# Kernel optimization log

Measured on AMD Instinct MI355X. Metric: run time of the kernel, lower is better.

Reference implementation:

```python
import jax, jax.numpy as jnp
import numpy as np

H = 56; W = 56; WS = 7; SHIFT = 3; HEADS = 4; DIM = 128
N = WS * WS  # 49 tokens per window
EPS = 1e-5


def _rel_pos_index():
    c = np.stack(np.meshgrid(np.arange(WS), np.arange(WS), indexing='ij')).reshape(2, -1)
    r = (c[:, :, None] - c[:, None, :]).transpose(1, 2, 0)
    r[..., 0] += WS - 1
    r[..., 1] += WS - 1
    r[..., 0] *= 2 * WS - 1
    return jnp.asarray(r.sum(-1))  # [N, N] int


def _attn_mask():
    img = np.zeros((H, W))
    sl = (slice(0, -WS), slice(-WS, -SHIFT), slice(-SHIFT, None))
    cnt = 0
    for hs in sl:
        for ws_ in sl:
            img[hs, ws_] = cnt
            cnt += 1
    mw = img.reshape(H // WS, WS, W // WS, WS).transpose(0, 2, 1, 3).reshape(-1, N)
    d = mw[:, None, :] - mw[:, :, None]  # [nW, N, N]
    return jnp.asarray(np.where(d != 0, -100.0, 0.0).astype(np.float32))


def _ln(x, w, b):
    m = x.mean(-1, keepdims=True)
    v = ((x - m) ** 2).mean(-1, keepdims=True)
    return (x - m) / jnp.sqrt(v + EPS) * w + b


def setup_inputs() -> dict:
    key = jax.random.key(0)
    ks = jax.random.split(key, 8)
    B = 64
    return {
        'x': jax.random.normal(ks[0], (B, H * W, DIM), jnp.float32),
        'qkv_w': jax.random.normal(ks[1], (DIM, 3 * DIM), jnp.float32) * 0.02,
        'qkv_b': jnp.zeros((3 * DIM,), jnp.float32),
        'proj_w': jax.random.normal(ks[2], (DIM, DIM), jnp.float32) * 0.02,
        'proj_b': jnp.zeros((DIM,), jnp.float32),
        'rpb_table': jax.random.normal(ks[3], ((2 * WS - 1) ** 2, HEADS), jnp.float32) * 0.02,
        'norm1_w': jnp.ones((DIM,), jnp.float32),
        'norm1_b': jnp.zeros((DIM,), jnp.float32),
        'norm2_w': jnp.ones((DIM,), jnp.float32),
        'norm2_b': jnp.zeros((DIM,), jnp.float32),
        'mlp_w1': jax.random.normal(ks[4], (DIM, 4 * DIM), jnp.float32) * 0.02,
        'mlp_b1': jnp.zeros((4 * DIM,), jnp.float32),
        'mlp_w2': jax.random.normal(ks[5], (4 * DIM, DIM), jnp.float32) * 0.02,
        'mlp_b2': jnp.zeros((DIM,), jnp.float32),
    }


def reference(x, qkv_w, qkv_b, proj_w, proj_b, rpb_table,
              norm1_w, norm1_b, norm2_w, norm2_b,
              mlp_w1, mlp_b1, mlp_w2, mlp_b2):
    B = x.shape[0]
    C = DIM
    hd = C // HEADS
    shortcut = x
    h = _ln(x, norm1_w, norm1_b).reshape(B, H, W, C)
    # cyclic shift
    h = jnp.roll(h, (-SHIFT, -SHIFT), axis=(1, 2))
    # window partition -> [B*nW, N, C]
    xw = h.reshape(B, H // WS, WS, W // WS, WS, C).transpose(0, 1, 3, 2, 4, 5).reshape(-1, N, C)
    qkv = (xw @ qkv_w + qkv_b).reshape(-1, N, 3, HEADS, hd).transpose(2, 0, 3, 1, 4)
    q, k, v = qkv[0] * (hd ** -0.5), qkv[1], qkv[2]  # [B*nW, heads, N, hd]
    attn = jnp.einsum('whnd,whmd->whnm', q, k)
    bias = rpb_table[_rel_pos_index().reshape(-1)].reshape(N, N, HEADS).transpose(2, 0, 1)
    attn = attn + bias[None]
    mask = _attn_mask()  # [nW, N, N]
    nW = mask.shape[0]
    attn = attn.reshape(B, nW, HEADS, N, N) + mask[None, :, None]
    attn = jax.nn.softmax(attn.reshape(-1, HEADS, N, N), axis=-1)
    out = jnp.einsum('whnm,whmd->wnhd', attn, v).reshape(-1, N, C)
    out = out @ proj_w + proj_b
    # window reverse + reverse shift
    out = out.reshape(B, H // WS, W // WS, WS, WS, C).transpose(0, 1, 3, 2, 4, 5).reshape(B, H, W, C)
    out = jnp.roll(out, (SHIFT, SHIFT), axis=(1, 2)).reshape(B, H * W, C)
    x = shortcut + out
    h2 = _ln(x, norm2_w, norm2_b)
    h2 = jax.nn.gelu(h2 @ mlp_w1 + mlp_b1, approximate=False) @ mlp_w2 + mlp_b2
    return x + h2
```

## Files before the change

### kernel.cpp

```cpp
#include <hip/hip_runtime.h>

#define HH 56
#define WW2 56
#define WS 7
#define SHIFT 3
#define HEADS 4
#define DIM 128
#define NTOK 49
#define BATCH 64
#define TOKENS (BATCH*HH*WW2)
#define NWIN 64
#define WINDOWS (BATCH*NWIN)

typedef __bf16 bf16x8 __attribute__((ext_vector_type(8)));
typedef float  f32x4  __attribute__((ext_vector_type(4)));

__device__ __forceinline__ unsigned short f2bf(float f) {
  union { __bf16 b; unsigned short u; } cv;
  cv.b = (__bf16)f;
  return cv.u;
}

__device__ __forceinline__ void st4(unsigned short* p, float a, float b, float c, float d) {
  ushort4 pk; pk.x = f2bf(a); pk.y = f2bf(b); pk.z = f2bf(c); pk.w = f2bf(d);
  *(ushort4*)p = pk;
}

__device__ __forceinline__ int reg3(int g) { return g >= 53 ? 2 : (g >= 49 ? 1 : 0); }

__global__ __launch_bounds__(256) void k_prep(
    const float* __restrict__ qkv_w, const float* __restrict__ proj_w,
    const float* __restrict__ w1, const float* __restrict__ w2,
    unsigned short* __restrict__ qkvwT, unsigned short* __restrict__ projwT,
    unsigned short* __restrict__ w1T, unsigned short* __restrict__ w2T)
{
  int idx = blockIdx.x * 256 + threadIdx.x;
  if (idx < 49152) {
    int n = idx >> 7, k = idx & 127;
    qkvwT[idx] = f2bf(qkv_w[k * 384 + n]);
  } else if (idx < 65536) {
    int i = idx - 49152; int n = i >> 7, k = i & 127;
    projwT[i] = f2bf(proj_w[k * 128 + n]);
  } else if (idx < 131072) {
    int i = idx - 65536; int n = i >> 7, k = i & 127;
    w1T[i] = f2bf(w1[k * 512 + n]);
  } else {
    int i = idx - 131072; int n = i >> 9, k = i & 511;
    w2T[i] = f2bf(w2[k * 128 + n]);
  }
}

__global__ __launch_bounds__(256) void k_tbl(const float* __restrict__ rpb, float* __restrict__ tbl)
{
  int idx = blockIdx.x * 256 + threadIdx.x;
  int kt = idx & 63, qt = (idx >> 6) & 63, h = (idx >> 12) & 3, cls = idx >> 14;
  float v;
  if (qt >= NTOK || kt >= NTOK) v = -3e38f;
  else {
    int qi = qt / 7, qj = qt % 7, ki = kt / 7, kj = kt % 7;
    int bi = (cls & 2) ? 49 : 0, bj = (cls & 1) ? 49 : 0;
    int rq = reg3(bi + qi) * 3 + reg3(bj + qj);
    int rk = reg3(bi + ki) * 3 + reg3(bj + kj);
    v = rpb[((qi - ki + 6) * 13 + (qj - kj + 6)) * HEADS + h] + (rq != rk ? -100.0f : 0.0f);
  }
  tbl[idx] = v;
}

__global__ __launch_bounds__(512, 4) void k_attn(
    const float* __restrict__ x,
    const float* __restrict__ n1w, const float* __restrict__ n1b,
    const unsigned short* __restrict__ qkvwT,
    const float* __restrict__ qkv_b,
    const unsigned short* __restrict__ projwT,
    const float* __restrict__ proj_b,
    const float* __restrict__ tbl,
    unsigned short* __restrict__ attn_out)
{
  __shared__ __align__(16) unsigned short s_x[64 * 136];
  __shared__ __align__(16) unsigned short s_qk[64 * 264];
  __shared__ __align__(16) unsigned short s_vT[128 * 72];

  int tid = threadIdx.x;
  int wave = tid >> 6;
  int lane = tid & 63;
  int l = lane & 15, g = lane >> 4;
  int win = blockIdx.x;
  int wi = (win & 63) >> 3, wj = win & 7;
  int bi = win >> 6;

  {
    float2 wv1 = *(const float2*)(n1w + lane * 2);
    float2 bv1 = *(const float2*)(n1b + lane * 2);
    float2 vr[7];
    #pragma unroll
    for (int rr = 0; rr < 7; ++rr) {
      int row = wave + rr * 8;
      if (row < NTOK) {
        int ti = row / 7, tj = row % 7;
        int i = wi * WS + ti + SHIFT; if (i >= HH) i -= HH;
        int j = wj * WS + tj + SHIFT; if (j >= WW2) j -= WW2;
        const float* xp = x + ((size_t)(bi * (HH * WW2) + i * WW2 + j)) * DIM;
        vr[rr] = *(const float2*)(xp + lane * 2);
      }
    }
    #pragma unroll
    for (int rr = 0; rr < 7; ++rr) {
      int row = wave + rr * 8;
      if (row < NTOK) {
        float2 v = vr[rr];
        float s = v.x + v.y, sq = v.x * v.x + v.y * v.y;
        #pragma unroll
        for (int off = 32; off; off >>= 1) {
          s += __shfl_xor(s, off);
          sq += __shfl_xor(sq, off);
        }
        float mean = s * (1.0f / DIM);
        float var = sq * (1.0f / DIM) - mean * mean;
        float rs = rsqrtf(var + 1e-5f);
        float y0 = (v.x - mean) * rs * wv1.x + bv1.x;
        float y1 = (v.y - mean) * rs * wv1.y + bv1.y;
        unsigned pack = ((unsigned)f2bf(y1) << 16) | (unsigned)f2bf(y0);
        *(unsigned*)&s_x[row * 136 + lane * 2] = pack;
      }
    }
  }
  for (int idx = tid; idx < 15 * 17; idx += 512) {
    int row = 49 + idx / 17, seg = idx % 17;
    *(uint4*)&s_x[row * 136 + seg * 8] = make_uint4(0, 0, 0, 0);
  }
  __syncthreads();

  bf16x8 xf[4][4];
  #pragma unroll
  for (int nt = 0; nt < 4; ++nt)
    #pragma unroll
    for (int kk = 0; kk < 4; ++kk)
      xf[nt][kk] = *(const bf16x8*)&s_x[(nt * 16 + l) * 136 + kk * 32 + g * 8];

  #pragma unroll
  for (int wti = 0; wti < 3; ++wti) {
    int wt = wave * 3 + wti;
    bf16x8 wf[4];
    #pragma unroll
    for (int kk = 0; kk < 4; ++kk)
      wf[kk] = *(const bf16x8*)(qkvwT + (size_t)(wt * 16 + l) * DIM + kk * 32 + g * 8);
    f32x4 acc[4];
    #pragma unroll
    for (int nt = 0; nt < 4; ++nt) acc[nt] = (f32x4){0.f, 0.f, 0.f, 0.f};
    #pragma unroll
    for (int kk = 0; kk < 4; ++kk)
      #pragma unroll
      for (int nt = 0; nt < 4; ++nt)
        acc[nt] = __builtin_amdgcn_mfma_f32_16x16x32_bf16(wf[kk], xf[nt][kk], acc[nt], 0, 0, 0);
    float4 b4 = *(const float4*)(qkv_b + wt * 16 + g * 4);
    if (wt < 16) {
      float sc = wt < 8 ? 0.17677669529663687f : 1.0f;
      #pragma unroll
      for (int nt = 0; nt < 4; ++nt)
        st4(&s_qk[(nt * 16 + l) * 264 + wt * 16 + g * 4],
            (acc[nt][0] + b4.x) * sc, (acc[nt][1] + b4.y) * sc,
            (acc[nt][2] + b4.z) * sc, (acc[nt][3] + b4.w) * sc);
    } else {
      int d0 = wt * 16 - 256 + g * 4;
      #pragma unroll
      for (int nt = 0; nt < 4; ++nt) {
        s_vT[(d0 + 0) * 72 + nt * 16 + l] = f2bf(acc[nt][0] + b4.x);
        s_vT[(d0 + 1) * 72 + nt * 16 + l] = f2bf(acc[nt][1] + b4.y);
        s_vT[(d0 + 2) * 72 + nt * 16 + l] = f2bf(acc[nt][2] + b4.z);
        s_vT[(d0 + 3) * 72 + nt * 16 + l] = f2bf(acc[nt][3] + b4.w);
      }
    }
  }
  __syncthreads();

  int h = wave >> 1, qh = wave & 1;
  bf16x8 kf[4], qf[2];
  #pragma unroll
  for (int mt = 0; mt < 4; ++mt)
    kf[mt] = *(const bf16x8*)&s_qk[(mt * 16 + l) * 264 + 128 + h * 32 + g * 8];
  #pragma unroll
  for (int nt2 = 0; nt2 < 2; ++nt2) {
    int nt = qh * 2 + nt2;
    qf[nt2] = *(const bf16x8*)&s_qk[(nt * 16 + l) * 264 + h * 32 + g * 8];
  }
  __syncthreads();

  int clsid = ((wi == 7) ? 2 : 0) | ((wj == 7) ? 1 : 0);
  const float* tb = tbl + ((clsid * 4 + h) << 12);
  f32x4 sc[4][2];
  #pragma unroll
  for (int nt2 = 0; nt2 < 2; ++nt2) {
    int nt = qh * 2 + nt2;
    #pragma unroll
    for (int mt = 0; mt < 4; ++mt) {
      f32x4 ci = *(const f32x4*)(tb + (nt * 16 + l) * 64 + mt * 16 + g * 4);
      sc[mt][nt2] = __builtin_amdgcn_mfma_f32_16x16x32_bf16(kf[mt], qf[nt2], ci, 0, 0, 0);
    }
  }

  #pragma unroll
  for (int nt2 = 0; nt2 < 2; ++nt2) {
    int nt = qh * 2 + nt2;
    float m = sc[0][nt2][0];
    #pragma unroll
    for (int mt = 0; mt < 4; ++mt)
      #pragma unroll
      for (int rr = 0; rr < 4; ++rr) m = fmaxf(m, sc[mt][nt2][rr]);
    m = fmaxf(m, __shfl_xor(m, 16));
    m = fmaxf(m, __shfl_xor(m, 32));
    float ssum = 0.f;
    #pragma unroll
    for (int mt = 0; mt < 4; ++mt)
      #pragma unroll
      for (int rr = 0; rr < 4; ++rr) {
        float e = __expf(sc[mt][nt2][rr] - m);
        sc[mt][nt2][rr] = e;
        ssum += e;
      }
    ssum += __shfl_xor(ssum, 16);
    ssum += __shfl_xor(ssum, 32);
    float inv = 1.0f / ssum;
    #pragma unroll
    for (int mt = 0; mt < 4; ++mt)
      st4(&s_qk[(nt * 16 + l) * 264 + h * 64 + mt * 16 + g * 4],
          sc[mt][nt2][0] * inv, sc[mt][nt2][1] * inv, sc[mt][nt2][2] * inv, sc[mt][nt2][3] * inv);
  }
  __syncthreads();

  int dt = qh;
  bf16x8 vf[2], pf[4][2];
  #pragma unroll
  for (int kk = 0; kk < 2; ++kk)
    vf[kk] = *(const bf16x8*)&s_vT[(h * 32 + dt * 16 + l) * 72 + kk * 32 + g * 8];
  #pragma unroll
  for (int nt = 0; nt < 4; ++nt)
    #pragma unroll
    for (int kk = 0; kk < 2; ++kk)
      pf[nt][kk] = *(const bf16x8*)&s_qk[(nt * 16 + l) * 264 + h * 64 + kk * 32 + g * 8];
  #pragma unroll
  for (int nt = 0; nt < 4; ++nt) {
    f32x4 a = (f32x4){0.f, 0.f, 0.f, 0.f};
    a = __builtin_amdgcn_mfma_f32_16x16x32_bf16(vf[0], pf[nt][0], a, 0, 0, 0);
    a = __builtin_amdgcn_mfma_f32_16x16x32_bf16(vf[1], pf[nt][1], a, 0, 0, 0);
    st4(&s_x[(nt * 16 + l) * 136 + h * 32 + dt * 16 + g * 4], a[0], a[1], a[2], a[3]);
  }
  __syncthreads();

  unsigned short* stage = s_vT;
  bf16x8 of[4][4];
  #pragma unroll
  for (int nt = 0; nt < 4; ++nt)
    #pragma unroll
    for (int kk = 0; kk < 4; ++kk)
      of[nt][kk] = *(const bf16x8*)&s_x[(nt * 16 + l) * 136 + kk * 32 + g * 8];
  {
    int wt = wave;
    bf16x8 wf[4];
    #pragma unroll
    for (int kk = 0; kk < 4; ++kk)
      wf[kk] = *(const bf16x8*)(projwT + (size_t)(wt * 16 + l) * DIM + kk * 32 + g * 8);
    f32x4 acc[4];
    #pragma unroll
    for (int nt = 0; nt < 4; ++nt) acc[nt] = (f32x4){0.f, 0.f, 0.f, 0.f};
    #pragma unroll
    for (int kk = 0; kk < 4; ++kk)
      #pragma unroll
      for (int nt = 0; nt < 4; ++nt)
        acc[nt] = __builtin_amdgcn_mfma_f32_16x16x32_bf16(wf[kk], of[nt][kk], acc[nt], 0, 0, 0);
    float4 b4 = *(const float4*)(proj_b + wt * 16 + g * 4);
    #pragma unroll
    for (int nt = 0; nt < 4; ++nt)
      st4(&stage[(nt * 16 + l) * 136 + wt * 16 + g * 4],
          acc[nt][0] + b4.x, acc[nt][1] + b4.y, acc[nt][2] + b4.z, acc[nt][3] + b4.w);
  }
  __syncthreads();

  unsigned short* outp = attn_out + (size_t)win * (NTOK * DIM);
  for (int idx = tid; idx < NTOK * 16; idx += 512) {
    int row = idx >> 4, seg = idx & 15;
    *(uint4*)(outp + idx * 8) = *(const uint4*)&stage[row * 136 + seg * 8];
  }
}

__device__ __forceinline__ float gelu_f(float x) {
  float x2 = x * x;
  float t = x * __builtin_fmaf(x2, -0.10294429f, -2.3022077f);
  float e = __builtin_amdgcn_exp2f(t);
  return x * __builtin_amdgcn_rcpf(1.0f + e);
}

__global__ __launch_bounds__(256) void k_mlp(
    const float* __restrict__ x, const unsigned short* __restrict__ attn,
    const float* __restrict__ n2w, const float* __restrict__ n2b,
    const unsigned short* __restrict__ w1T, const float* __restrict__ b1,
    const unsigned short* __restrict__ w2T, const float* __restrict__ b2,
    float* __restrict__ io)
{
  __shared__ __align__(16) unsigned short s_t[2][64 * 136];
  __shared__ float s_part[64][4][2];
  int tid = threadIdx.x;
  int wave = tid >> 6;
  int lane = tid & 63;
  int l = lane & 15, g = lane >> 4;
  size_t m0 = (size_t)blockIdx.x * 64;
  int col0 = wave * 32 + g * 4;

  float4 xz[4][2];
  float sA[4], sQ[4];
  #pragma unroll
  for (int nt = 0; nt < 4; ++nt) {
    int row = nt * 16 + l;
    int t = (int)m0 + row;
    int bi = t / (HH * WW2);
    int r = t % (HH * WW2);
    int i = r / WW2, j = r % WW2;
    int si = i >= SHIFT ? i - SHIFT : i + (HH - SHIFT);
    int sj = j >= SHIFT ? j - SHIFT : j + (WW2 - SHIFT);
    int win = bi * NWIN + (si / WS) * 8 + (sj / WS);
    int tok = (si % WS) * WS + (sj % WS);
    const float* xp = x + (size_t)t * DIM;
    const unsigned short* ap = attn + ((size_t)(win * NTOK + tok)) * DIM;
    float s = 0.f, sq = 0.f;
    #pragma unroll
    for (int wti = 0; wti < 2; ++wti) {
      int col = col0 + wti * 16;
      float4 xv = *(const float4*)(xp + col);
      ushort4 av = *(const ushort4*)(ap + col);
      float4 z;
      z.x = xv.x + __uint_as_float((unsigned)av.x << 16);
      z.y = xv.y + __uint_as_float((unsigned)av.y << 16);
      z.z = xv.z + __uint_as_float((unsigned)av.z << 16);
      z.w = xv.w + __uint_as_float((unsigned)av.w << 16);
      xz[nt][wti] = z;
      s += z.x + z.y + z.z + z.w;
      sq += z.x * z.x + z.y * z.y + z.z * z.z + z.w * z.w;
    }
    s += __shfl_xor(s, 16); s += __shfl_xor(s, 32);
    sq += __shfl_xor(sq, 16); sq += __shfl_xor(sq, 32);
    sA[nt] = s; sQ[nt] = sq;
  }
  if (g == 0) {
    #pragma unroll
    for (int nt = 0; nt < 4; ++nt) {
      s_part[nt * 16 + l][wave][0] = sA[nt];
      s_part[nt * 16 + l][wave][1] = sQ[nt];
    }
  }
  __syncthreads();
  float4 wv0 = *(const float4*)(n2w + col0);
  float4 wv1 = *(const float4*)(n2w + col0 + 16);
  float4 bv0 = *(const float4*)(n2b + col0);
  float4 bv1 = *(const float4*)(n2b + col0 + 16);
  #pragma unroll
  for (int nt = 0; nt < 4; ++nt) {
    int row = nt * 16 + l;
    float s = 0.f, sq = 0.f;
    #pragma unroll
    for (int wv = 0; wv < 4; ++wv) { s += s_part[row][wv][0]; sq += s_part[row][wv][1]; }
    float mean = s * (1.0f / DIM);
    float var = sq * (1.0f / DIM) - mean * mean;
    float rs = rsqrtf(var + 1e-5f);
    float4 z0 = xz[nt][0], z1 = xz[nt][1];
    st4(&s_t[1][row * 136 + col0],
        (z0.x - mean) * rs * wv0.x + bv0.x, (z0.y - mean) * rs * wv0.y + bv0.y,
        (z0.z - mean) * rs * wv0.z + bv0.z, (z0.w - mean) * rs * wv0.w + bv0.w);
    st4(&s_t[1][row * 136 + col0 + 16],
        (z1.x - mean) * rs * wv1.x + bv1.x, (z1.y - mean) * rs * wv1.y + bv1.y,
        (z1.z - mean) * rs * wv1.z + bv1.z, (z1.w - mean) * rs * wv1.w + bv1.w);
  }
  __syncthreads();

  bf16x8 hf[4][4];
  #pragma unroll
  for (int nt = 0; nt < 4; ++nt)
    #pragma unroll
    for (int kk = 0; kk < 4; ++kk)
      hf[nt][kk] = *(const bf16x8*)&s_t[1][(nt * 16 + l) * 136 + kk * 32 + g * 8];

  f32x4 o[2][4];
  #pragma unroll
  for (int wti = 0; wti < 2; ++wti)
    #pragma unroll
    for (int nt = 0; nt < 4; ++nt) o[wti][nt] = (f32x4){0.f, 0.f, 0.f, 0.f};

  for (int c = 0; c < 4; ++c) {
    unsigned short* buf = s_t[c & 1];
    #pragma unroll
    for (int wti = 0; wti < 2; ++wti) {
      int wt = wave * 2 + wti;
      int n0 = c * 128 + wt * 16;
      bf16x8 wf[4];
      #pragma unroll
      for (int kk = 0; kk < 4; ++kk)
        wf[kk] = *(const bf16x8*)(w1T + (size_t)(n0 + l) * DIM + kk * 32 + g * 8);
      f32x4 acc[4];
      #pragma unroll
      for (int nt = 0; nt < 4; ++nt) acc[nt] = (f32x4){0.f, 0.f, 0.f, 0.f};
      #pragma unroll
      for (int kk = 0; kk < 4; ++kk)
        #pragma unroll
        for (int nt = 0; nt < 4; ++nt)
          acc[nt] = __builtin_amdgcn_mfma_f32_16x16x32_bf16(wf[kk], hf[nt][kk], acc[nt], 0, 0, 0);
      float4 b4 = *(const float4*)(b1 + n0 + g * 4);
      #pragma unroll
      for (int nt = 0; nt < 4; ++nt)
        st4(&buf[(nt * 16 + l) * 136 + wt * 16 + g * 4],
            gelu_f(acc[nt][0] + b4.x), gelu_f(acc[nt][1] + b4.y),
            gelu_f(acc[nt][2] + b4.z), gelu_f(acc[nt][3] + b4.w));
    }
    __syncthreads();
    #pragma unroll
    for (int kk = 0; kk < 4; ++kk) {
      bf16x8 tf[4];
      #pragma unroll
      for (int nt = 0; nt < 4; ++nt)
        tf[nt] = *(const bf16x8*)&buf[(nt * 16 + l) * 136 + kk * 32 + g * 8];
      #pragma unroll
      for (int wti = 0; wti < 2; ++wti) {
        int wt = wave * 2 + wti;
        bf16x8 wf2 = *(const bf16x8*)(w2T + (size_t)(wt * 16 + l) * 512 + c * 128 + kk * 32 + g * 8);
        #pragma unroll
        for (int nt = 0; nt < 4; ++nt)
          o[wti][nt] = __builtin_amdgcn_mfma_f32_16x16x32_bf16(wf2, tf[nt], o[wti][nt], 0, 0, 0);
      }
    }
  }

  #pragma unroll
  for (int wti = 0; wti < 2; ++wti) {
    int wt = wave * 2 + wti;
    float4 b4 = *(const float4*)(b2 + wt * 16 + g * 4);
    #pragma unroll
    for (int nt = 0; nt < 4; ++nt) {
      float4 z = xz[nt][wti];
      float4 pv;
      pv.x = z.x + o[wti][nt][0] + b4.x;
      pv.y = z.y + o[wti][nt][1] + b4.y;
      pv.z = z.z + o[wti][nt][2] + b4.z;
      pv.w = z.w + o[wti][nt][3] + b4.w;
      *(float4*)(io + (m0 + nt * 16 + l) * DIM + wt * 16 + g * 4) = pv;
    }
  }
}

extern "C" void kernel_launch(void* const* d_in, const int* in_sizes, int n_in,
                              void* d_out, int out_size, void* d_ws, size_t ws_size,
                              hipStream_t stream) {
  const float* x       = (const float*)d_in[0];
  const float* qkv_w   = (const float*)d_in[1];
  const float* qkv_b   = (const float*)d_in[2];
  const float* proj_w  = (const float*)d_in[3];
  const float* proj_b  = (const float*)d_in[4];
  const float* rpb     = (const float*)d_in[5];
  const float* n1w     = (const float*)d_in[6];
  const float* n1b     = (const float*)d_in[7];
  const float* n2w     = (const float*)d_in[8];
  const float* n2b     = (const float*)d_in[9];
  const float* mlp_w1  = (const float*)d_in[10];
  const float* mlp_b1  = (const float*)d_in[11];
  const float* mlp_w2  = (const float*)d_in[12];
  const float* mlp_b2  = (const float*)d_in[13];
  float* out = (float*)d_out;

  char* ws = (char*)d_ws;
  const size_t TOKB = (size_t)TOKENS * DIM * 2;
  unsigned short* attn_o = (unsigned short*)(ws);
  unsigned short* qkvwT  = (unsigned short*)(ws + TOKB);
  unsigned short* projwT = (unsigned short*)(ws + TOKB + 98304);
  unsigned short* w1T    = (unsigned short*)(ws + TOKB + 98304 + 32768);
  unsigned short* w2T    = (unsigned short*)(ws + TOKB + 98304 + 32768 + 131072);
  float*          tbl    = (float*)(ws + TOKB + 98304 + 32768 + 131072 + 131072);

  k_prep<<<768, 256, 0, stream>>>(qkv_w, proj_w, mlp_w1, mlp_w2, qkvwT, projwT, w1T, w2T);
  k_tbl<<<256, 256, 0, stream>>>(rpb, tbl);
  k_attn<<<WINDOWS, 512, 0, stream>>>(x, n1w, n1b, qkvwT, qkv_b, projwT, proj_b, tbl, attn_o);
  k_mlp<<<TOKENS / 64, 256, 0, stream>>>(x, attn_o, n2w, n2b, w1T, mlp_b1, w2T, mlp_b2, out);
}
```

Baseline: 444.8 us.

## Split MLP kernel work across 8 waves per block instead of 4

```diff
diff --git a/kernel.cpp b/kernel.cpp
--- a/kernel.cpp
+++ b/kernel.cpp
@@ -289,7 +289,7 @@
   return x * __builtin_amdgcn_rcpf(1.0f + e);
 }
 
-__global__ __launch_bounds__(256) void k_mlp(
+__global__ __launch_bounds__(512, 4) void k_mlp(
     const float* __restrict__ x, const unsigned short* __restrict__ attn,
     const float* __restrict__ n2w, const float* __restrict__ n2b,
     const unsigned short* __restrict__ w1T, const float* __restrict__ b1,
@@ -297,15 +297,15 @@
     float* __restrict__ io)
 {
   __shared__ __align__(16) unsigned short s_t[2][64 * 136];
-  __shared__ float s_part[64][4][2];
+  __shared__ float s_part[64][8][2];
   int tid = threadIdx.x;
   int wave = tid >> 6;
   int lane = tid & 63;
   int l = lane & 15, g = lane >> 4;
   size_t m0 = (size_t)blockIdx.x * 64;
-  int col0 = wave * 32 + g * 4;
-
-  float4 xz[4][2];
+  int col0 = wave * 16 + g * 4;
+
+  float4 xz[4];
   float sA[4], sQ[4];
   #pragma unroll
   for (int nt = 0; nt < 4; ++nt) {
@@ -318,23 +318,16 @@
     int sj = j >= SHIFT ? j - SHIFT : j + (WW2 - SHIFT);
     int win = bi * NWIN + (si / WS) * 8 + (sj / WS);
     int tok = (si % WS) * WS + (sj % WS);
-    const float* xp = x + (size_t)t * DIM;
-    const unsigned short* ap = attn + ((size_t)(win * NTOK + tok)) * DIM;
-    float s = 0.f, sq = 0.f;
-    #pragma unroll
-    for (int wti = 0; wti < 2; ++wti) {
-      int col = col0 + wti * 16;
-      float4 xv = *(const float4*)(xp + col);
-      ushort4 av = *(const ushort4*)(ap + col);
-      float4 z;
-      z.x = xv.x + __uint_as_float((unsigned)av.x << 16);
-      z.y = xv.y + __uint_as_float((unsigned)av.y << 16);
-      z.z = xv.z + __uint_as_float((unsigned)av.z << 16);
-      z.w = xv.w + __uint_as_float((unsigned)av.w << 16);
-      xz[nt][wti] = z;
-      s += z.x + z.y + z.z + z.w;
-      sq += z.x * z.x + z.y * z.y + z.z * z.z + z.w * z.w;
-    }
+    float4 xv = *(const float4*)(x + (size_t)t * DIM + col0);
+    ushort4 av = *(const ushort4*)(attn + ((size_t)(win * NTOK + tok)) * DIM + col0);
+    float4 z;
+    z.x = xv.x + __uint_as_float((unsigned)av.x << 16);
+    z.y = xv.y + __uint_as_float((unsigned)av.y << 16);
+    z.z = xv.z + __uint_as_float((unsigned)av.z << 16);
+    z.w = xv.w + __uint_as_float((unsigned)av.w << 16);
+    xz[nt] = z;
+    float s = z.x + z.y + z.z + z.w;
+    float sq = z.x * z.x + z.y * z.y + z.z * z.z + z.w * z.w;
     s += __shfl_xor(s, 16); s += __shfl_xor(s, 32);
     sq += __shfl_xor(sq, 16); sq += __shfl_xor(sq, 32);
     sA[nt] = s; sQ[nt] = sq;
@@ -348,25 +341,20 @@
   }
   __syncthreads();
   float4 wv0 = *(const float4*)(n2w + col0);
-  float4 wv1 = *(const float4*)(n2w + col0 + 16);
   float4 bv0 = *(const float4*)(n2b + col0);
-  float4 bv1 = *(const float4*)(n2b + col0 + 16);
   #pragma unroll
   for (int nt = 0; nt < 4; ++nt) {
     int row = nt * 16 + l;
     float s = 0.f, sq = 0.f;
     #pragma unroll
-    for (int wv = 0; wv < 4; ++wv) { s += s_part[row][wv][0]; sq += s_part[row][wv][1]; }
+    for (int wv = 0; wv < 8; ++wv) { s += s_part[row][wv][0]; sq += s_part[row][wv][1]; }
     float mean = s * (1.0f / DIM);
     float var = sq * (1.0f / DIM) - mean * mean;
     float rs = rsqrtf(var + 1e-5f);
-    float4 z0 = xz[nt][0], z1 = xz[nt][1];
+    float4 z0 = xz[nt];
     st4(&s_t[1][row * 136 + col0],
         (z0.x - mean) * rs * wv0.x + bv0.x, (z0.y - mean) * rs * wv0.y + bv0.y,
         (z0.z - mean) * rs * wv0.z + bv0.z, (z0.w - mean) * rs * wv0.w + bv0.w);
-    st4(&s_t[1][row * 136 + col0 + 16],
-        (z1.x - mean) * rs * wv1.x + bv1.x, (z1.y - mean) * rs * wv1.y + bv1.y,
-        (z1.z - mean) * rs * wv1.z + bv1.z, (z1.w - mean) * rs * wv1.w + bv1.w);
   }
   __syncthreads();
 
@@ -377,18 +365,14 @@
     for (int kk = 0; kk < 4; ++kk)
       hf[nt][kk] = *(const bf16x8*)&s_t[1][(nt * 16 + l) * 136 + kk * 32 + g * 8];
 
-  f32x4 o[2][4];
-  #pragma unroll
-  for (int wti = 0; wti < 2; ++wti)
-    #pragma unroll
-    for (int nt = 0; nt < 4; ++nt) o[wti][nt] = (f32x4){0.f, 0.f, 0.f, 0.f};
+  f32x4 o[4];
+  #pragma unroll
+  for (int nt = 0; nt < 4; ++nt) o[nt] = (f32x4){0.f, 0.f, 0.f, 0.f};
 
   for (int c = 0; c < 4; ++c) {
     unsigned short* buf = s_t[c & 1];
-    #pragma unroll
-    for (int wti = 0; wti < 2; ++wti) {
-      int wt = wave * 2 + wti;
-      int n0 = c * 128 + wt * 16;
+    {
+      int n0 = c * 128 + wave * 16;
       bf16x8 wf[4];
       #pragma unroll
       for (int kk = 0; kk < 4; ++kk)
@@ -404,7 +388,7 @@
       float4 b4 = *(const float4*)(b1 + n0 + g * 4);
       #pragma unroll
       for (int nt = 0; nt < 4; ++nt)
-        st4(&buf[(nt * 16 + l) * 136 + wt * 16 + g * 4],
+        st4(&buf[(nt * 16 + l) * 136 + wave * 16 + g * 4],
             gelu_f(acc[nt][0] + b4.x), gelu_f(acc[nt][1] + b4.y),
             gelu_f(acc[nt][2] + b4.z), gelu_f(acc[nt][3] + b4.w));
     }
@@ -415,30 +399,24 @@
       #pragma unroll
       for (int nt = 0; nt < 4; ++nt)
         tf[nt] = *(const bf16x8*)&buf[(nt * 16 + l) * 136 + kk * 32 + g * 8];
-      #pragma unroll
-      for (int wti = 0; wti < 2; ++wti) {
-        int wt = wave * 2 + wti;
-        bf16x8 wf2 = *(const bf16x8*)(w2T + (size_t)(wt * 16 + l) * 512 + c * 128 + kk * 32 + g * 8);
-        #pragma unroll
-        for (int nt = 0; nt < 4; ++nt)
-          o[wti][nt] = __builtin_amdgcn_mfma_f32_16x16x32_bf16(wf2, tf[nt], o[wti][nt], 0, 0, 0);
-      }
-    }
-  }
-
-  #pragma unroll
-  for (int wti = 0; wti < 2; ++wti) {
-    int wt = wave * 2 + wti;
-    float4 b4 = *(const float4*)(b2 + wt * 16 + g * 4);
+      bf16x8 wf2 = *(const bf16x8*)(w2T + (size_t)(wave * 16 + l) * 512 + c * 128 + kk * 32 + g * 8);
+      #pragma unroll
+      for (int nt = 0; nt < 4; ++nt)
+        o[nt] = __builtin_amdgcn_mfma_f32_16x16x32_bf16(wf2, tf[nt], o[nt], 0, 0, 0);
+    }
+  }
+
+  {
+    float4 b4 = *(const float4*)(b2 + col0);
     #pragma unroll
     for (int nt = 0; nt < 4; ++nt) {
-      float4 z = xz[nt][wti];
+      float4 z = xz[nt];
       float4 pv;
-      pv.x = z.x + o[wti][nt][0] + b4.x;
-      pv.y = z.y + o[wti][nt][1] + b4.y;
-      pv.z = z.z + o[wti][nt][2] + b4.z;
-      pv.w = z.w + o[wti][nt][3] + b4.w;
-      *(float4*)(io + (m0 + nt * 16 + l) * DIM + wt * 16 + g * 4) = pv;
+      pv.x = z.x + o[nt][0] + b4.x;
+      pv.y = z.y + o[nt][1] + b4.y;
+      pv.z = z.z + o[nt][2] + b4.z;
+      pv.w = z.w + o[nt][3] + b4.w;
+      *(float4*)(io + (m0 + nt * 16 + l) * DIM + col0) = pv;
     }
   }
 }
@@ -474,5 +452,5 @@
   k_prep<<<768, 256, 0, stream>>>(qkv_w, proj_w, mlp_w1, mlp_w2, qkvwT, projwT, w1T, w2T);
   k_tbl<<<256, 256, 0, stream>>>(rpb, tbl);
   k_attn<<<WINDOWS, 512, 0, stream>>>(x, n1w, n1b, qkvwT, qkv_b, projwT, proj_b, tbl, attn_o);
-  k_mlp<<<TOKENS / 64, 256, 0, stream>>>(x, attn_o, n2w, n2b, w1T, mlp_b1, w2T, mlp_b2, out);
-}
+  k_mlp<<<TOKENS / 64, 512, 0, stream>>>(x, attn_o, n2w, n2b, w1T, mlp_b1, w2T, mlp_b2, out);
+}
```

Result: slower. 495.1 us (+11.3%).
